# Optimization experiments

Measured on AMD Instinct MI355X. Metric: run time of the kernel, lower is better.

## Reference

```python
import jax, jax.numpy as jnp
import numpy as np

T, B, IN, H, OUT = 2048, 512, 27, 64, 26
EPS = 1e-5
DROP = 0.1


def setup_inputs() -> dict:
    key = jax.random.key(0)
    ks = jax.random.split(key, 11)
    s = 1.0 / np.sqrt(H)
    u = lambda k, shape: jax.random.uniform(k, shape, jnp.float32, -s, s)
    return {
        "obscure_word": jax.random.normal(ks[0], (T, B, IN), jnp.float32),
        "prev_guess": jax.random.uniform(ks[1], (T, OUT), jnp.float32),
        "W_ih": u(ks[2], (4 * H, IN)),
        "W_hh": u(ks[3], (4 * H, H)),
        "b_ih": u(ks[4], (4 * H,)),
        "b_hh": u(ks[5], (4 * H,)),
        "gamma": jnp.ones((H,), jnp.float32),
        "beta": jnp.zeros((H,), jnp.float32),
        "W_fc": u(ks[6], (OUT, H + OUT)),
        "b_fc": u(ks[7], (OUT,)),
        # LockedDropout mask: sampled once, reused every timestep, pre-scaled by 1/(1-p)
        "drop_mask": (jax.random.uniform(ks[8], (B, H)) < (1.0 - DROP)).astype(jnp.float32) / (1.0 - DROP),
    }


def reference(obscure_word, prev_guess, W_ih, W_hh, b_ih, b_hh, gamma, beta, W_fc, b_fc, drop_mask):
    h0 = jnp.zeros((B, H), obscure_word.dtype)
    c0 = jnp.zeros((B, H), obscure_word.dtype)

    def step(carry, inputs):
        h, c = carry
        x_t, pg_t = inputs  # [B, IN], [OUT]
        gates = x_t @ W_ih.T + b_ih + h @ W_hh.T + b_hh  # [B, 4H]
        i, f, g, o = jnp.split(gates, 4, axis=1)
        i = jax.nn.sigmoid(i)
        f = jax.nn.sigmoid(f)
        g = jnp.tanh(g)
        o = jax.nn.sigmoid(o)
        c_new = f * c + i * g
        h_new = o * jnp.tanh(c_new)
        # BatchNorm1d (training mode: per-timestep batch stats, biased var)
        mean = jnp.mean(h_new, axis=0)
        var = jnp.mean((h_new - mean) ** 2, axis=0)
        hb = (h_new - mean) * jax.lax.rsqrt(var + EPS) * gamma + beta
        # LockedDropout (same mask every timestep)
        hd = hb * drop_mask
        # MaxPool1d over batch dim -> [H]
        pooled = jnp.max(hd, axis=0)
        out = jnp.concatenate([pooled, pg_t])  # [H+OUT]
        y = out @ W_fc.T + b_fc  # [OUT]
        return (h_new, c_new), y

    _, ys = jax.lax.scan(step, (h0, c0), (obscure_word, prev_guess))
    return ys[:, None, :]  # [T, 1, OUT]
```

## Files before the change

kernel.cpp:

```cpp
#include <hip/hip_runtime.h>
#include <hip/hip_bf16.h>

#define TT   2048
#define BB   512
#define IN_  27
#define HH   64
#define NG   256
#define OUTD 26
#define EPSV 1e-5f

__device__ __forceinline__ float bcastf(float v, int lane) {
    return __int_as_float(__builtin_amdgcn_readlane(__float_as_int(v), lane));
}

__device__ __forceinline__ float sigm(float x) {
    return 1.0f / (1.0f + __expf(-x));
}

__device__ __forceinline__ float tanh_fast(float x) {
    float e = __expf(-2.0f * fabsf(x));
    float r = (1.0f - e) / (1.0f + e);
    return copysignf(r, x);
}

__global__ __launch_bounds__(256, 2) void lstm_seq(
    const float* __restrict__ x,
    const float* __restrict__ W_ih,
    const float* __restrict__ W_hh,
    const float* __restrict__ b_ih,
    const float* __restrict__ b_hh,
    float* __restrict__ h_all,
    float* __restrict__ state,
    int t0, int tc, int first)
{
    const int b = blockIdx.x;
    const int j = threadIdx.x;
    const int q = j >> 6;
    const int l = j & 63;

    float wi[IN_];
#pragma unroll
    for (int k = 0; k < IN_; ++k) wi[k] = W_ih[j * IN_ + k];
    float wh[HH];
#pragma unroll
    for (int k = 0; k < HH; ++k) wh[k] = W_hh[j * HH + k];
    const float bias = b_ih[j] + b_hh[j];

    float hv, cv;
    if (first) {
        hv = 0.0f; cv = 0.0f;
    } else {
        hv = state[b * HH + l];
        cv = state[BB * HH + b * HH + l];
    }

    __shared__ float acts[2][NG];

    for (int tl = 0; tl < tc; ++tl) {
        const int t = t0 + tl;

        float xv = 0.0f;
        if (l < IN_) xv = x[((size_t)t * BB + b) * IN_ + l];

        float a0 = bias, a1 = 0.0f, a2 = 0.0f, a3 = 0.0f;
#pragma unroll
        for (int k = 0; k < HH; k += 4) {
            a0 = fmaf(bcastf(hv, k + 0), wh[k + 0], a0);
            a1 = fmaf(bcastf(hv, k + 1), wh[k + 1], a1);
            a2 = fmaf(bcastf(hv, k + 2), wh[k + 2], a2);
            a3 = fmaf(bcastf(hv, k + 3), wh[k + 3], a3);
        }
#pragma unroll
        for (int k = 0; k < 24; k += 4) {
            a0 = fmaf(bcastf(xv, k + 0), wi[k + 0], a0);
            a1 = fmaf(bcastf(xv, k + 1), wi[k + 1], a1);
            a2 = fmaf(bcastf(xv, k + 2), wi[k + 2], a2);
            a3 = fmaf(bcastf(xv, k + 3), wi[k + 3], a3);
        }
        a0 = fmaf(bcastf(xv, 24), wi[24], a0);
        a1 = fmaf(bcastf(xv, 25), wi[25], a1);
        a2 = fmaf(bcastf(xv, 26), wi[26], a2);
        const float acc = (a0 + a1) + (a2 + a3);

        const float av = (q == 2) ? tanh_fast(acc) : sigm(acc);

        acts[tl & 1][j] = av;
        __syncthreads();

        const float gi = acts[tl & 1][l];
        const float gf = acts[tl & 1][HH + l];
        const float gg = acts[tl & 1][2 * HH + l];
        const float go = acts[tl & 1][3 * HH + l];

        const float cn = fmaf(gf, cv, gi * gg);
        const float hn = go * tanh_fast(cn);
        cv = cn;
        hv = hn;

        if (q == 0) h_all[((size_t)tl * BB + b) * HH + l] = hn;
    }

    if (q == 0) {
        state[b * HH + l] = hv;
        state[BB * HH + b * HH + l] = cv;
    }
}

__global__ __launch_bounds__(256, 2) void bn_pool_fc(
    const float* __restrict__ h_all,
    const float* __restrict__ gamma,
    const float* __restrict__ beta,
    const float* __restrict__ dmask,
    const float* __restrict__ pg,
    const float* __restrict__ W_fc,
    const float* __restrict__ b_fc,
    float* __restrict__ y,
    int t0, int tc)
{
    const int tl = blockIdx.x;
    const int t = t0 + tl;
    const int tid = threadIdx.x;
    const int g = tid >> 6;
    const int hcol = tid & 63;
    const float* hp = h_all + (size_t)tl * BB * HH;

    __shared__ float s_a[4][HH];
    __shared__ float s_b[4][HH];
    __shared__ float s_scale[HH];
    __shared__ float s_shift[HH];
    __shared__ float s_pool[HH];

    float sum = 0.0f, sq = 0.0f;
    for (int bb = g; bb < BB; bb += 4) {
        const float v = hp[bb * HH + hcol];
        sum += v;
        sq = fmaf(v, v, sq);
    }
    s_a[g][hcol] = sum;
    s_b[g][hcol] = sq;
    __syncthreads();

    if (tid < HH) {
        const float s  = (s_a[0][tid] + s_a[1][tid]) + (s_a[2][tid] + s_a[3][tid]);
        const float q2 = (s_b[0][tid] + s_b[1][tid]) + (s_b[2][tid] + s_b[3][tid]);
        const float mean = s * (1.0f / BB);
        const float var  = q2 * (1.0f / BB) - mean * mean;
        const float rs = rsqrtf(var + EPSV);
        const float sc = rs * gamma[tid];
        s_scale[tid] = sc;
        s_shift[tid] = beta[tid] - mean * sc;
    }
    __syncthreads();

    const float sc = s_scale[hcol];
    const float sh = s_shift[hcol];
    float m = -3.0e38f;
    for (int bb = g; bb < BB; bb += 4) {
        const float v = hp[bb * HH + hcol];
        const float hd = fmaf(v, sc, sh) * dmask[bb * HH + hcol];
        m = fmaxf(m, hd);
    }
    s_a[g][hcol] = m;
    __syncthreads();
    if (tid < HH) {
        s_pool[tid] = fmaxf(fmaxf(s_a[0][tid], s_a[1][tid]),
                            fmaxf(s_a[2][tid], s_a[3][tid]));
    }
    __syncthreads();

    if (tid < OUTD) {
        float acc = b_fc[tid];
        const float* w = W_fc + tid * (HH + OUTD);
#pragma unroll
        for (int k = 0; k < HH; ++k) acc = fmaf(w[k], s_pool[k], acc);
#pragma unroll
        for (int k = 0; k < OUTD; ++k) acc = fmaf(w[HH + k], pg[t * OUTD + k], acc);
        y[t * OUTD + tid] = acc;
    }
}

extern "C" void kernel_launch(void* const* d_in, const int* in_sizes, int n_in,
                              void* d_out, int out_size, void* d_ws, size_t ws_size,
                              hipStream_t stream)
{
    const float* x     = (const float*)d_in[0];
    const float* pg    = (const float*)d_in[1];
    const float* W_ih  = (const float*)d_in[2];
    const float* W_hh  = (const float*)d_in[3];
    const float* b_ih  = (const float*)d_in[4];
    const float* b_hh  = (const float*)d_in[5];
    const float* gamma = (const float*)d_in[6];
    const float* beta  = (const float*)d_in[7];
    const float* W_fc  = (const float*)d_in[8];
    const float* b_fc  = (const float*)d_in[9];
    const float* dmask = (const float*)d_in[10];
    float* y = (float*)d_out;

    const size_t state_bytes = 2ull * BB * HH * sizeof(float);
    const size_t per_t = (size_t)BB * HH * sizeof(float);
    size_t avail = (ws_size > state_bytes) ? (ws_size - state_bytes) : 0;
    int chunkT = (int)(avail / per_t);
    if (chunkT > TT) chunkT = TT;
    if (chunkT < 1) chunkT = 1;

    float* h_all = (float*)d_ws;
    float* state = (float*)((char*)d_ws + (size_t)chunkT * per_t);

    int first = 1;
    for (int t0 = 0; t0 < TT; t0 += chunkT) {
        int tc = TT - t0;
        if (tc > chunkT) tc = chunkT;
        lstm_seq<<<BB, 256, 0, stream>>>(x, W_ih, W_hh, b_ih, b_hh,
                                         h_all, state, t0, tc, first);
        bn_pool_fc<<<tc, 256, 0, stream>>>(h_all, gamma, beta, dmask, pg,
                                           W_fc, b_fc, y, t0, tc);
        first = 0;
    }
}
```

Measured before the change: 2.244 ms.

## Run each batch row's LSTM in one wavefront, dropping per-step LDS barrier

The LSTM recurrence now runs one 64-lane wavefront per batch row instead of a 256-thread block. Each lane computes all four gates for its hidden unit, using 364 register-held weights. This removes the shared-memory gate exchange and the __syncthreads on every timestep, and the next step's input is prefetched one step ahead. In exchange, the serial FMA chain per lane grows fourfold and register pressure is high, with a risk of spills. Only 512 wavefronts are in flight, so latency hiding relies on one wave per SIMD.

```diff
diff --git a/kernel.cpp b/kernel.cpp
--- a/kernel.cpp
+++ b/kernel.cpp
@@ -1,11 +1,9 @@
 #include <hip/hip_runtime.h>
-#include <hip/hip_bf16.h>
 
 #define TT   2048
 #define BB   512
 #define IN_  27
 #define HH   64
-#define NG   256
 #define OUTD 26
 #define EPSV 1e-5f
 
@@ -23,7 +21,7 @@
     return copysignf(r, x);
 }
 
-__global__ __launch_bounds__(256, 2) void lstm_seq(
+__global__ __launch_bounds__(64, 1) void lstm_seq(
     const float* __restrict__ x,
     const float* __restrict__ W_ih,
     const float* __restrict__ W_hh,
@@ -34,17 +32,20 @@
     int t0, int tc, int first)
 {
     const int b = blockIdx.x;
-    const int j = threadIdx.x;
-    const int q = j >> 6;
-    const int l = j & 63;
-
-    float wi[IN_];
-#pragma unroll
-    for (int k = 0; k < IN_; ++k) wi[k] = W_ih[j * IN_ + k];
-    float wh[HH];
-#pragma unroll
-    for (int k = 0; k < HH; ++k) wh[k] = W_hh[j * HH + k];
-    const float bias = b_ih[j] + b_hh[j];
+    const int l = threadIdx.x;
+
+    float wi[4][IN_];
+    float wh[4][HH];
+    float bias[4];
+#pragma unroll
+    for (int q = 0; q < 4; ++q) {
+        const int j = q * HH + l;
+#pragma unroll
+        for (int k = 0; k < IN_; ++k) wi[q][k] = W_ih[j * IN_ + k];
+#pragma unroll
+        for (int k = 0; k < HH; ++k) wh[q][k] = W_hh[j * HH + k];
+        bias[q] = b_ih[j] + b_hh[j];
+    }
 
     float hv, cv;
     if (first) {
@@ -54,56 +55,48 @@
         cv = state[BB * HH + b * HH + l];
     }
 
-    __shared__ float acts[2][NG];
-
+    float xv = (l < IN_) ? x[((size_t)t0 * BB + b) * IN_ + l] : 0.0f;
+
+#pragma unroll 1
     for (int tl = 0; tl < tc; ++tl) {
         const int t = t0 + tl;
 
-        float xv = 0.0f;
-        if (l < IN_) xv = x[((size_t)t * BB + b) * IN_ + l];
-
-        float a0 = bias, a1 = 0.0f, a2 = 0.0f, a3 = 0.0f;
-#pragma unroll
-        for (int k = 0; k < HH; k += 4) {
-            a0 = fmaf(bcastf(hv, k + 0), wh[k + 0], a0);
-            a1 = fmaf(bcastf(hv, k + 1), wh[k + 1], a1);
-            a2 = fmaf(bcastf(hv, k + 2), wh[k + 2], a2);
-            a3 = fmaf(bcastf(hv, k + 3), wh[k + 3], a3);
+        const float xcur = xv;
+        int tn = t + 1; if (tn > TT - 1) tn = TT - 1;
+        xv = (l < IN_) ? x[((size_t)tn * BB + b) * IN_ + l] : 0.0f;
+
+        float a0 = bias[0], a1 = bias[1], a2 = bias[2], a3 = bias[3];
+
+#pragma unroll
+        for (int k = 0; k < HH; ++k) {
+            const float hk = bcastf(hv, k);
+            a0 = fmaf(hk, wh[0][k], a0);
+            a1 = fmaf(hk, wh[1][k], a1);
+            a2 = fmaf(hk, wh[2][k], a2);
+            a3 = fmaf(hk, wh[3][k], a3);
         }
 #pragma unroll
-        for (int k = 0; k < 24; k += 4) {
-            a0 = fmaf(bcastf(xv, k + 0), wi[k + 0], a0);
-            a1 = fmaf(bcastf(xv, k + 1), wi[k + 1], a1);
-            a2 = fmaf(bcastf(xv, k + 2), wi[k + 2], a2);
-            a3 = fmaf(bcastf(xv, k + 3), wi[k + 3], a3);
+        for (int k = 0; k < IN_; ++k) {
+            const float xk = bcastf(xcur, k);
+            a0 = fmaf(xk, wi[0][k], a0);
+            a1 = fmaf(xk, wi[1][k], a1);
+            a2 = fmaf(xk, wi[2][k], a2);
+            a3 = fmaf(xk, wi[3][k], a3);
         }
-        a0 = fmaf(bcastf(xv, 24), wi[24], a0);
-        a1 = fmaf(bcastf(xv, 25), wi[25], a1);
-        a2 = fmaf(bcastf(xv, 26), wi[26], a2);
-        const float acc = (a0 + a1) + (a2 + a3);
-
-        const float av = (q == 2) ? tanh_fast(acc) : sigm(acc);
-
-        acts[tl & 1][j] = av;
-        __syncthreads();
-
-        const float gi = acts[tl & 1][l];
-        const float gf = acts[tl & 1][HH + l];
-        const float gg = acts[tl & 1][2 * HH + l];
-        const float go = acts[tl & 1][3 * HH + l];
-
-        const float cn = fmaf(gf, cv, gi * gg);
-        const float hn = go * tanh_fast(cn);
-        cv = cn;
-        hv = hn;
-
-        if (q == 0) h_all[((size_t)tl * BB + b) * HH + l] = hn;
-    }
-
-    if (q == 0) {
-        state[b * HH + l] = hv;
-        state[BB * HH + b * HH + l] = cv;
-    }
+
+        const float gi = sigm(a0);
+        const float gf = sigm(a1);
+        const float gg = tanh_fast(a2);
+        const float go = sigm(a3);
+
+        cv = fmaf(gf, cv, gi * gg);
+        hv = go * tanh_fast(cv);
+
+        h_all[((size_t)tl * BB + b) * HH + l] = hv;
+    }
+
+    state[b * HH + l] = hv;
+    state[BB * HH + b * HH + l] = cv;
 }
 
 __global__ __launch_bounds__(256, 2) void bn_pool_fc(
@@ -210,8 +203,8 @@
     for (int t0 = 0; t0 < TT; t0 += chunkT) {
         int tc = TT - t0;
         if (tc > chunkT) tc = chunkT;
-        lstm_seq<<<BB, 256, 0, stream>>>(x, W_ih, W_hh, b_ih, b_hh,
-                                         h_all, state, t0, tc, first);
+        lstm_seq<<<BB, 64, 0, stream>>>(x, W_ih, W_hh, b_ih, b_hh,
+                                        h_all, state, t0, tc, first);
         bn_pool_fc<<<tc, 256, 0, stream>>>(h_all, gamma, beta, dmask, pg,
                                            W_fc, b_fc, y, t0, tc);
         first = 0;
```

Result: slower. 3.133 ms (+39.6%).
